# Optimization experiments

Measured on AMD Instinct MI355X. Metric: run time of the kernel, lower is better.

The kernel has to match this reference:

```python
import jax, jax.numpy as jnp
import numpy as np

N, F_IN, F_OUT = 8192, 512, 256


def setup_inputs() -> dict:
    key = jax.random.key(0)
    k1, k2, k3, k4 = jax.random.split(key, 4)
    x = jax.random.normal(k1, (N, F_IN), dtype=jnp.float32)
    adj = jax.random.randint(k2, (N, N), 0, 2, dtype=jnp.int32)
    # xavier-uniform-like init scale for W and a
    wb = 1.414 * np.sqrt(6.0 / (F_IN + F_OUT))
    ab = 1.414 * np.sqrt(6.0 / (2 * F_OUT + 1))
    W = jax.random.uniform(k3, (F_IN, F_OUT), minval=-wb, maxval=wb, dtype=jnp.float32)
    a = jax.random.uniform(k4, (2 * F_OUT, 1), minval=-ab, maxval=ab, dtype=jnp.float32)
    return {"x": x, "adj": adj, "W": W, "a": a, "heads": 4}


def reference(x, adj, W, a, heads):
    # Wh = x @ W : [N, F_OUT]
    Wh = x @ W
    f_out = W.shape[1]
    # a = [a_src; a_dst], so e_ij = leakyrelu(Wh_i . a_src + Wh_j . a_dst)
    s_src = Wh @ a[:f_out, 0]   # [N]
    s_dst = Wh @ a[f_out:, 0]   # [N]
    e = jax.nn.leaky_relu(s_src[:, None] + s_dst[None, :], negative_slope=0.2)  # [N, N]
    # scatter into dense matrix: non-edges hold 0 and DO participate in softmax
    att = jnp.where(adj != 0, e, jnp.zeros((), dtype=e.dtype))
    att = jax.nn.softmax(att, axis=1)
    # dropout is identity in eval mode (self.training=False)
    h = att @ Wh                                  # [N, F_OUT]
    n = x.shape[0]
    h = h.reshape(n, heads, f_out // heads).mean(axis=1)  # multi-head mean
    return h
```

## Files before the change

kernel.cpp:

```cpp
#include <hip/hip_runtime.h>
#include <hip/hip_bf16.h>

#define NN 8192
#define FIN 512
#define FOUT 256
#define FH 64
#define JSPLIT 32
#define JCHUNK (NN / JSPLIT)
#define STEPS (JCHUNK / 32)

typedef float f32x16 __attribute__((ext_vector_type(16)));
typedef short bf16x8 __attribute__((ext_vector_type(8)));
typedef unsigned short us8 __attribute__((ext_vector_type(8)));
typedef unsigned int uint32x4 __attribute__((ext_vector_type(4)));

static __device__ __forceinline__ unsigned short f2bf(float x) {
  unsigned int u = __builtin_bit_cast(unsigned int, x);
  unsigned int r = (u + 0x7fffu + ((u >> 16) & 1u)) >> 16;
  return (unsigned short)r;
}
static __device__ __forceinline__ float bf2f(unsigned short u) {
  unsigned int v = ((unsigned int)u) << 16;
  return __builtin_bit_cast(float, v);
}
static __device__ __forceinline__ float fastexp2(float x) {
  float r;
  asm("v_exp_f32 %0, %1" : "=v"(r) : "v"(x));
  return r;
}
static __device__ __forceinline__ unsigned int pkbf(float a, float b) {
  unsigned int w;
  asm("v_cvt_pk_bf16_f32 %0, %1, %2" : "=v"(w) : "v"(a), "v"(b));
  return w;
}
static __device__ __forceinline__ float lo16f(unsigned int w) {
  return __builtin_bit_cast(float, w << 16);
}
static __device__ __forceinline__ float hi16f(unsigned int w) {
  return __builtin_bit_cast(float, w & 0xffff0000u);
}
static __device__ __forceinline__ unsigned int ext4(int l31,
    unsigned long long c0, unsigned long long c1,
    unsigned long long c2, unsigned long long c3) {
  unsigned long long s01 = (l31 & 8) ? c1 : c0;
  unsigned long long s23 = (l31 & 8) ? c3 : c2;
  unsigned long long s = (l31 & 16) ? s23 : s01;
  return (unsigned int)(s >> ((l31 & 7) * 8)) & 0xffu;
}

__global__ __launch_bounds__(256) void prep_small(const float* __restrict__ W,
                                                  const float* __restrict__ a,
                                                  unsigned short* __restrict__ Bw) {
  const int kt = blockIdx.x;
  __shared__ float wm[16][64];
  __shared__ float wt[16][2];
  const int t = threadIdx.x;
#pragma unroll
  for (int i = 0; i < 4; ++i) {
    const int idx = t + i * 256;
    const int kr = idx >> 6, c = idx & 63;
    const float* wr = W + (size_t)(kt * 16 + kr) * FOUT + c;
    wm[kr][c] = 0.25f * (wr[0] + wr[64] + wr[128] + wr[192]);
  }
  if (t < 32) {
    const int kr = t & 15, sel = t >> 4;
    const float* wr = W + (size_t)(kt * 16 + kr) * FOUT;
    const float* av = a + sel * FOUT;
    float s = 0.f;
    for (int n = 0; n < FOUT; ++n) s += wr[n] * av[n];
    wt[kr][sel] = s * 1.44269504f;
  }
  __syncthreads();
#pragma unroll
  for (int i = 0; i < 12; ++i) {
    const int idx = t + i * 256;
    const int e = idx & 7, n = (idx >> 3) & 31, r2 = idx >> 8;
    const int khb = r2 & 1, q = r2 >> 1;
    const int nf = q % 3, h = q / 3;
    const int k = khb * 8 + e;
    float v = nf < 2 ? wm[k][nf * 32 + n]
                     : (n == 0 ? wt[k][0] : (n == 1 ? wt[k][1] : 0.f));
    const unsigned short hi = f2bf(v);
    Bw[(size_t)kt * 3072 + idx] = (h == 0) ? hi : f2bf(v - bf2f(hi));
  }
}

__global__ __launch_bounds__(192) void gemm_whm(const float* __restrict__ X,
                                                const unsigned short* __restrict__ Bw,
                                                unsigned short* __restrict__ Bg,
                                                float* __restrict__ ssrc,
                                                float* __restrict__ sdst) {
  __shared__ float xs[32][516];
  __shared__ float sred[32][2];
  const int mw = blockIdx.x;
  const int tid = threadIdx.x;
  const float* xb = X + (size_t)(mw * 32) * FIN;
  for (int i = tid; i < 4096; i += 192) {
    const int row = i >> 7, c4 = (i & 127) << 2;
    *(float4*)&xs[row][c4] = *(const float4*)(xb + (size_t)row * FIN + c4);
  }
  __syncthreads();

  const int nf = tid >> 6, lane = tid & 63;
  const int l31 = lane & 31, kh = lane >> 5;
  f32x16 acc = (f32x16)(0.f);
  const unsigned short* bp = Bw + ((size_t)nf * 2 + kh) * 256 + l31 * 8;
#pragma unroll 4
  for (int kt = 0; kt < 32; ++kt) {
    const float* xr = &xs[l31][kt * 16 + kh * 8];
    const float4 va = *(const float4*)xr;
    const float4 vb = *(const float4*)(xr + 4);
    const unsigned int h0 = pkbf(va.x, va.y), h1 = pkbf(va.z, va.w);
    const unsigned int h2 = pkbf(vb.x, vb.y), h3 = pkbf(vb.z, vb.w);
    const unsigned int l0 = pkbf(va.x - lo16f(h0), va.y - hi16f(h0));
    const unsigned int l1 = pkbf(va.z - lo16f(h1), va.w - hi16f(h1));
    const unsigned int l2 = pkbf(vb.x - lo16f(h2), vb.y - hi16f(h2));
    const unsigned int l3 = pkbf(vb.z - lo16f(h3), vb.w - hi16f(h3));
    const uint32x4 uh = {h0, h1, h2, h3}, ul = {l0, l1, l2, l3};
    const bf16x8 a_h = __builtin_bit_cast(bf16x8, uh);
    const bf16x8 a_l = __builtin_bit_cast(bf16x8, ul);
    const bf16x8 b_h = *(const bf16x8*)(bp + kt * 3072);
    const bf16x8 b_l = *(const bf16x8*)(bp + kt * 3072 + 1536);
    acc = __builtin_amdgcn_mfma_f32_32x32x16_bf16(a_h, b_h, acc, 0, 0, 0);
    acc = __builtin_amdgcn_mfma_f32_32x32x16_bf16(a_h, b_l, acc, 0, 0, 0);
    acc = __builtin_amdgcn_mfma_f32_32x32x16_bf16(a_l, b_h, acc, 0, 0, 0);
  }
  if (nf < 2) {
    unsigned short* bgw = Bg + (size_t)mw * 2048;
#pragma unroll
    for (int reg = 0; reg < 16; reg += 2) {
      const unsigned int wh = pkbf(acc[reg], acc[reg + 1]);
      const int e = (reg & 3) | (kh << 2);
      const int khb = (reg >> 2) & 1;
      const int kc = reg >> 3;
      *(unsigned int*)(bgw + (size_t)(((kc * 2 + khb) * 2 + nf) * 256) +
                       l31 * 8 + e) = wh;
    }
  } else if (l31 < 2) {
#pragma unroll
    for (int reg = 0; reg < 16; ++reg) {
      const int row = (reg & 3) + ((reg >> 2) << 3) + (kh << 2);
      sred[row][l31] = acc[reg];
    }
  }
  __syncthreads();
  if (threadIdx.x < 32) {
    ssrc[mw * 32 + threadIdx.x] = sred[threadIdx.x][0];
    sdst[mw * 32 + threadIdx.x] = sred[threadIdx.x][1];
  }
}

#define GLL(G, L)                                                           \
  __builtin_amdgcn_global_load_lds(                                         \
      (const __attribute__((address_space(1))) unsigned int*)(G),           \
      (__attribute__((address_space(3))) unsigned int*)(L), 16, 0, 0)

#define PEL(P, MM, B, SD)                    \
  float P;                                   \
  {                                          \
    float tt = ss + (SD);                    \
    float lr = fmaxf(tt, 0.2f * tt);         \
    lr = (((MM) >> (B)) & 1u) ? lr : 0.0f;   \
    P = fastexp2(lr);                        \
    dacc += P;                               \
  }

#define GENAF(AF, M0, M1, M2, M3, KC4, SA, SB)                            \
  {                                                                       \
    PEL(p0, M0, (KC4) + 0, (SA).x) PEL(p1, M1, (KC4) + 0, (SA).y)         \
    PEL(p2, M2, (KC4) + 0, (SA).z) PEL(p3, M3, (KC4) + 0, (SA).w)         \
    PEL(p4, M0, (KC4) + 1, (SB).x) PEL(p5, M1, (KC4) + 1, (SB).y)         \
    PEL(p6, M2, (KC4) + 1, (SB).z) PEL(p7, M3, (KC4) + 1, (SB).w)         \
    const uint32x4 uv = {pkbf(p0, p1), pkbf(p2, p3), pkbf(p4, p5),        \
                         pkbf(p6, p7)};                                   \
    AF = __builtin_bit_cast(bf16x8, uv);                                  \
  }

__global__ __launch_bounds__(512, 4) void gat_aggr(
    const int* __restrict__ adj, const float* __restrict__ ssrc_g,
    const float* __restrict__ sdst_g, const unsigned short* __restrict__ Bg,
    unsigned short* __restrict__ Upb, float* __restrict__ Dp) {
  __shared__ unsigned short lbuf[STEPS * 2048];
  __shared__ float sds[256];
  const int bid = blockIdx.x;
  const int bj = bid & 31, bm = bid >> 5;
  const int wv = threadIdx.x >> 6, lane = threadIdx.x & 63;
  const int l31 = lane & 31, kh = lane >> 5;
  const int rbase = bm * 256;
  const int myrow = rbase + wv * 32 + l31;
  const int jb = bj * JCHUNK;
  const float ss = ssrc_g[myrow];

  {
    const unsigned short* gs = Bg + (size_t)bj * (STEPS * 2048) +
                               (size_t)(wv * 4) * 512 + lane * 8;
#pragma unroll
    for (int c = 0; c < 4; ++c) GLL(gs + c * 512, &lbuf[(wv * 4 + c) * 512]);
    if (wv == 0) GLL(sdst_g + jb + lane * 4, &sds[0]);
  }

  const int* astep = adj + (size_t)(rbase + wv * 32 + (lane >> 3)) * NN + jb +
                     (lane & 7) * 4;
  int4 qa0 = *(const int4*)(astep + (size_t)0 * 8 * NN);
  int4 qa1 = *(const int4*)(astep + (size_t)1 * 8 * NN);
  int4 qa2 = *(const int4*)(astep + (size_t)2 * 8 * NN);
  int4 qa3 = *(const int4*)(astep + (size_t)3 * 8 * NN);
  int4 qb0 = *(const int4*)(astep + (size_t)0 * 8 * NN + 32);
  int4 qb1 = *(const int4*)(astep + (size_t)1 * 8 * NN + 32);
  int4 qb2 = *(const int4*)(astep + (size_t)2 * 8 * NN + 32);
  int4 qb3 = *(const int4*)(astep + (size_t)3 * 8 * NN + 32);

  f32x16 acc0 = (f32x16)(0.f), acc1 = (f32x16)(0.f);
  float dacc = 0.f;
  __syncthreads();

  const unsigned short* lb0 = &lbuf[kh * 512 + l31 * 8];
  const float* sdl = &sds[kh * 8];
  const int kh2 = kh * 2;

#define PSTEP(T, QS0, QS1, QS2, QS3, RELOAD)                                  \
  {                                                                          \
    const unsigned int mk0 = ext4(l31, __ballot((QS0).x != 0),               \
        __ballot((QS1).x != 0), __ballot((QS2).x != 0), __ballot((QS3).x != 0)); \
    const unsigned int mk1 = ext4(l31, __ballot((QS0).y != 0),               \
        __ballot((QS1).y != 0), __ballot((QS2).y != 0), __ballot((QS3).y != 0)); \
    const unsigned int mk2 = ext4(l31, __ballot((QS0).z != 0),               \
        __ballot((QS1).z != 0), __ballot((QS2).z != 0), __ballot((QS3).z != 0)); \
    const unsigned int mk3 = ext4(l31, __ballot((QS0).w != 0),               \
        __ballot((QS1).w != 0), __ballot((QS2).w != 0), __ballot((QS3).w != 0)); \
    if (RELOAD) {                                                            \
      const int* an = astep + ((T) + 2) * 32;                                \
      QS0 = *(const int4*)(an + (size_t)0 * 8 * NN);                         \
      QS1 = *(const int4*)(an + (size_t)1 * 8 * NN);                         \
      QS2 = *(const int4*)(an + (size_t)2 * 8 * NN);                         \
      QS3 = *(const int4*)(an + (size_t)3 * 8 * NN);                         \
    }                                                                        \
    const unsigned int m0 = mk0 >> kh2, m1 = mk1 >> kh2;                     \
    const unsigned int m2 = mk2 >> kh2, m3 = mk3 >> kh2;                     \
    const unsigned short* tb = lb0 + (size_t)(T) * 2048;                     \
    const bf16x8 b00 = *(const bf16x8*)(tb);                    \
    const bf16x8 b01 = *(const bf16x8*)(tb + 256);              \
    const bf16x8 b10 = *(const bf16x8*)(tb + 1024);             \
    const bf16x8 b11 = *(const bf16x8*)(tb + 1280);             \
    const float4 sA0 = *(const float4*)(sdl + (T) * 32);                     \
    const float4 sB0 = *(const float4*)(sdl + (T) * 32 + 4);                 \
    const float4 sA1 = *(const float4*)(sdl + (T) * 32 + 16);                \
    const float4 sB1 = *(const float4*)(sdl + (T) * 32 + 20);                \
    bf16x8 af0, af1;                                                         \
    GENAF(af0, m0, m1, m2, m3, 0, sA0, sB0)                                  \
    GENAF(af1, m0, m1, m2, m3, 4, sA1, sB1)                                  \
    acc0 = __builtin_amdgcn_mfma_f32_32x32x16_bf16(af0, b00, acc0, 0, 0, 0); \
    acc1 = __builtin_amdgcn_mfma_f32_32x32x16_bf16(af0, b01, acc1, 0, 0, 0); \
    acc0 = __builtin_amdgcn_mfma_f32_32x32x16_bf16(af1, b10, acc0, 0, 0, 0); \
    acc1 = __builtin_amdgcn_mfma_f32_32x32x16_bf16(af1, b11, acc1, 0, 0, 0); \
  }

#pragma unroll 1
  for (int it = 0; it < 3; ++it) {
    const int t0 = 2 * it;
    PSTEP(t0, qa0, qa1, qa2, qa3, 1)
    PSTEP(t0 + 1, qb0, qb1, qb2, qb3, 1)
  }
  PSTEP(6, qa0, qa1, qa2, qa3, 0)
  PSTEP(7, qb0, qb1, qb2, qb3, 0)
#undef PSTEP

  dacc += __shfl_xor(dacc, 32);
  if (lane < 32) Dp[(size_t)bj * NN + myrow] = dacc;

  unsigned short* ub = Upb + ((size_t)bj * NN + rbase + wv * 32) * FH;
#pragma unroll
  for (int reg = 0; reg < 16; ++reg) {
    const int rr = (reg & 3) + ((reg >> 2) << 3) + (kh << 2);
    ub[(size_t)rr * FH + l31] = f2bf(acc0[reg]);
    ub[(size_t)rr * FH + 32 + l31] = f2bf(acc1[reg]);
  }
}

__global__ __launch_bounds__(256) void finalize(const unsigned short* __restrict__ Upb,
                                                const float* __restrict__ Dp,
                                                float* __restrict__ out) {
  const int idx = blockIdx.x * 256 + threadIdx.x;
  const int i = idx >> 6;
  float u = 0.f, d = 0.f;
#pragma unroll
  for (int s = 0; s < JSPLIT; ++s) {
    d += Dp[(size_t)s * NN + i];
    u += bf2f(Upb[(size_t)s * NN * FH + idx]);
  }
  out[idx] = u / d;
}

extern "C" void kernel_launch(void* const* d_in, const int* in_sizes, int n_in,
                              void* d_out, int out_size, void* d_ws, size_t ws_size,
                              hipStream_t stream) {
  const float* x = (const float*)d_in[0];
  const int* adj = (const int*)d_in[1];
  const float* W = (const float*)d_in[2];
  const float* a = (const float*)d_in[3];
  char* ws = (char*)d_ws;

  unsigned short* Upb = (unsigned short*)ws;
  unsigned short* Bg = (unsigned short*)(ws + ((size_t)32 << 20));
  unsigned short* Bw = (unsigned short*)(ws + ((size_t)36 << 20));
  float* ssrc = (float*)(ws + ((size_t)36 << 20) + (256u << 10));
  float* sdst = (float*)(ws + ((size_t)36 << 20) + (288u << 10));
  float* Dp = (float*)(ws + ((size_t)36 << 20) + (320u << 10));
  float* out = (float*)d_out;

  prep_small<<<32, 256, 0, stream>>>(W, a, Bw);
  gemm_whm<<<256, 192, 0, stream>>>(x, Bw, Bg, ssrc, sdst);
  gat_aggr<<<32 * JSPLIT, 512, 0, stream>>>(adj, ssrc, sdst, Bg, Upb, Dp);
  finalize<<<NN * FH / 256, 256, 0, stream>>>(Upb, Dp, out);
}
```

Before: 91.05 us.

## Halve column splits by using 1024-thread blocks with in-block LDS reduction

The aggregation kernel now covers a 512-column chunk per block with 16 waves: two groups of 8 waves each take half the columns and are combined through shared memory before writing. This halves the number of partial U/D slices written to global memory and later summed by finalize, cutting partial-result traffic. In exchange it adds two block barriers and an LDS reduction, doubles the LDS footprint to about 67KB, and caps occupancy at one 1024-thread block per group of CUs. Finalize still loops over JSPLIT, which is now 16.

```diff
diff --git a/kernel.cpp b/kernel.cpp
--- a/kernel.cpp
+++ b/kernel.cpp
@@ -5,9 +5,9 @@
 #define FIN 512
 #define FOUT 256
 #define FH 64
-#define JSPLIT 32
-#define JCHUNK (NN / JSPLIT)
-#define STEPS (JCHUNK / 32)
+#define JSPLIT 16
+#define JCHUNK 512
+#define STEPS 8
 
 typedef float f32x16 __attribute__((ext_vector_type(16)));
 typedef short bf16x8 __attribute__((ext_vector_type(8)));
@@ -176,30 +176,34 @@
     AF = __builtin_bit_cast(bf16x8, uv);                                  \
   }
 
-__global__ __launch_bounds__(512, 4) void gat_aggr(
+__global__ __launch_bounds__(1024, 4) void gat_aggr(
     const int* __restrict__ adj, const float* __restrict__ ssrc_g,
     const float* __restrict__ sdst_g, const unsigned short* __restrict__ Bg,
     unsigned short* __restrict__ Upb, float* __restrict__ Dp) {
-  __shared__ unsigned short lbuf[STEPS * 2048];
-  __shared__ float sds[256];
+  __shared__ unsigned short lbuf[16 * 2048];
+  __shared__ float sds[768];
   const int bid = blockIdx.x;
-  const int bj = bid & 31, bm = bid >> 5;
+  const int bj = bid & 15, bm = bid >> 4;
   const int wv = threadIdx.x >> 6, lane = threadIdx.x & 63;
+  const int wvr = wv & 7, jhalf = wv >> 3;
   const int l31 = lane & 31, kh = lane >> 5;
   const int rbase = bm * 256;
-  const int myrow = rbase + wv * 32 + l31;
-  const int jb = bj * JCHUNK;
+  const int myrow = rbase + wvr * 32 + l31;
+  const int jb = bj * JCHUNK + jhalf * 256;
   const float ss = ssrc_g[myrow];
 
   {
-    const unsigned short* gs = Bg + (size_t)bj * (STEPS * 2048) +
-                               (size_t)(wv * 4) * 512 + lane * 8;
-#pragma unroll
-    for (int c = 0; c < 4; ++c) GLL(gs + c * 512, &lbuf[(wv * 4 + c) * 512]);
-    if (wv == 0) GLL(sdst_g + jb + lane * 4, &sds[0]);
-  }
-
-  const int* astep = adj + (size_t)(rbase + wv * 32 + (lane >> 3)) * NN + jb +
+    const unsigned short* gs =
+        Bg + (size_t)(bj * 16 + wv) * 2048 + lane * 8;
+#pragma unroll
+    for (int c = 0; c < 4; ++c) GLL(gs + c * 512, &lbuf[wv * 2048 + c * 512]);
+    if (wv == 0) {
+      GLL(sdst_g + bj * JCHUNK + lane * 4, &sds[0]);
+      GLL(sdst_g + bj * JCHUNK + 256 + lane * 4, &sds[256]);
+    }
+  }
+
+  const int* astep = adj + (size_t)(rbase + wvr * 32 + (lane >> 3)) * NN + jb +
                      (lane & 7) * 4;
   int4 qa0 = *(const int4*)(astep + (size_t)0 * 8 * NN);
   int4 qa1 = *(const int4*)(astep + (size_t)1 * 8 * NN);
@@ -214,8 +218,8 @@
   float dacc = 0.f;
   __syncthreads();
 
-  const unsigned short* lb0 = &lbuf[kh * 512 + l31 * 8];
-  const float* sdl = &sds[kh * 8];
+  const unsigned short* lb0 = &lbuf[(jhalf * 8) * 2048 + kh * 512 + l31 * 8];
+  const float* sdl = &sds[jhalf * 256 + kh * 8];
   const int kh2 = kh * 2;
 
 #define PSTEP(T, QS0, QS1, QS2, QS3, RELOAD)                                  \
@@ -266,9 +270,27 @@
 #undef PSTEP
 
   dacc += __shfl_xor(dacc, 32);
+  __syncthreads();
+  float* lf = (float*)lbuf;
+  const int slot = wvr * 2048;
+  if (jhalf) {
+#pragma unroll
+    for (int r = 0; r < 16; ++r) lf[slot + r * 64 + lane] = acc0[r];
+#pragma unroll
+    for (int r = 0; r < 16; ++r) lf[slot + (16 + r) * 64 + lane] = acc1[r];
+    if (lane < 32) sds[512 + wvr * 32 + l31] = dacc;
+  }
+  __syncthreads();
+  if (jhalf) return;
+#pragma unroll
+  for (int r = 0; r < 16; ++r) acc0[r] += lf[slot + r * 64 + lane];
+#pragma unroll
+  for (int r = 0; r < 16; ++r) acc1[r] += lf[slot + (16 + r) * 64 + lane];
+  dacc += sds[512 + wvr * 32 + l31];
+
   if (lane < 32) Dp[(size_t)bj * NN + myrow] = dacc;
 
-  unsigned short* ub = Upb + ((size_t)bj * NN + rbase + wv * 32) * FH;
+  unsigned short* ub = Upb + ((size_t)bj * NN + rbase + wvr * 32) * FH;
 #pragma unroll
   for (int reg = 0; reg < 16; ++reg) {
     const int rr = (reg & 3) + ((reg >> 2) << 3) + (kh << 2);
@@ -310,6 +332,6 @@
 
   prep_small<<<32, 256, 0, stream>>>(W, a, Bw);
   gemm_whm<<<256, 192, 0, stream>>>(x, Bw, Bg, ssrc, sdst);
-  gat_aggr<<<32 * JSPLIT, 512, 0, stream>>>(adj, ssrc, sdst, Bg, Upb, Dp);
+  gat_aggr<<<32 * JSPLIT, 1024, 0, stream>>>(adj, ssrc, sdst, Bg, Upb, Dp);
   finalize<<<NN * FH / 256, 256, 0, stream>>>(Upb, Dp, out);
 }
```

Result: faster. 83.52 us (-8.3%).
